# Kernel optimization log

Measured on AMD Instinct MI355X. Metric: run time of the kernel, lower is better.

## Reference

```python
import jax, jax.numpy as jnp
import numpy as np

B, T, IN, H, L, OUT = 1024, 48, 64, 512, 3, 1


def setup_inputs() -> dict:
    key = jax.random.key(0)
    ks = jax.random.split(key, 12)
    s = 0.05
    inp = {
        "x": jax.random.normal(ks[0], (B, T, IN), dtype=jnp.float32),
        # layer 0: input IN -> H ; gates concatenated [f,i,c,o] along last dim
        "Wx0": jax.random.normal(ks[1], (IN, 4 * H), dtype=jnp.float32) * s,
        "Wh0": jax.random.normal(ks[2], (H, 4 * H), dtype=jnp.float32) * s,
        "b0": jnp.zeros((4 * H,), dtype=jnp.float32),
        "Wx1": jax.random.normal(ks[3], (H, 4 * H), dtype=jnp.float32) * s,
        "Wh1": jax.random.normal(ks[4], (H, 4 * H), dtype=jnp.float32) * s,
        "b1": jnp.zeros((4 * H,), dtype=jnp.float32),
        "Wx2": jax.random.normal(ks[5], (H, 4 * H), dtype=jnp.float32) * s,
        "Wh2": jax.random.normal(ks[6], (H, 4 * H), dtype=jnp.float32) * s,
        "b2": jnp.zeros((4 * H,), dtype=jnp.float32),
        "fc_w": jax.random.normal(ks[7], (H, OUT), dtype=jnp.float32) * s,
        "fc_b": jnp.zeros((OUT,), dtype=jnp.float32),
    }
    return inp


def _lstm_cell(Wx, Wh, b, x_t, h, C):
    # fused 4-gate GEMM, same math as 8 separate Linears in the torch code
    g = x_t @ Wx + h @ Wh + b  # [B, 4H]
    f, i, c, o = jnp.split(g, 4, axis=-1)
    f = jax.nn.sigmoid(f)
    i = jax.nn.sigmoid(i)
    c = jnp.tanh(c)
    o = jax.nn.sigmoid(o)
    C_new = f * C + i * c
    h_new = o * jnp.tanh(C_new)  # dropout is identity in eval mode
    return h_new, C_new


def reference(x, Wx0, Wh0, b0, Wx1, Wh1, b1, Wx2, Wh2, b2, fc_w, fc_b):
    params = [(Wx0, Wh0, b0), (Wx1, Wh1, b1), (Wx2, Wh2, b2)]
    Bsz = x.shape[0]
    Hsz = Wh0.shape[0]
    h0 = jnp.zeros((L, Bsz, Hsz), dtype=x.dtype)
    C0 = jnp.zeros((L, Bsz, Hsz), dtype=x.dtype)

    def step(carry, x_t):
        h, C = carry
        inp = x_t
        hs, Cs = [], []
        for l in range(L):
            Wx, Wh, b = params[l]
            hn, Cn = _lstm_cell(Wx, Wh, b, inp, h[l], C[l])
            hs.append(hn)
            Cs.append(Cn)
            inp = hn
        return (jnp.stack(hs), jnp.stack(Cs)), None

    (h, C), _ = jax.lax.scan(step, (h0, C0), jnp.swapaxes(x, 0, 1))
    return h[-1] @ fc_w + fc_b  # [B, OUT]
```

## Files before the change

### kernel.cpp

```cpp
#include <hip/hip_runtime.h>
#include <hip/hip_bf16.h>
#include <stdint.h>

#define BSZ 1024
#define HSZ 512
#define TSZ 48
#define INSZ 64
#define GSZ 2048

typedef __attribute__((ext_vector_type(8))) short bf16x8;
typedef __attribute__((ext_vector_type(16))) float f32x16;

#define GLDS16(g, l)                                                        \
    __builtin_amdgcn_global_load_lds(                                       \
        (const __attribute__((address_space(1))) void*)(g),                 \
        (__attribute__((address_space(3))) void*)(l), 16, 0, 0)

#define SB0 __builtin_amdgcn_sched_barrier(0);
#define WAITV8 asm volatile("s_waitcnt vmcnt(8)" ::: "memory");
#define BARRAW __builtin_amdgcn_s_barrier();

__device__ __forceinline__ float sigmf(float x) { return 1.0f / (1.0f + __expf(-x)); }
__device__ __forceinline__ float tanhf_(float x) { return 2.0f / (1.0f + __expf(-2.0f * x)) - 1.0f; }

__global__ __launch_bounds__(256, 3) void lstm_diag(
    const __hip_bfloat16* __restrict__ xth, const __hip_bfloat16* __restrict__ xtl,
    __hip_bfloat16* __restrict__ hbuf,
    float* __restrict__ Cbuf,
    const __hip_bfloat16* __restrict__ W0h, const __hip_bfloat16* __restrict__ W0l,
    const __hip_bfloat16* __restrict__ W1h, const __hip_bfloat16* __restrict__ W1l,
    const __hip_bfloat16* __restrict__ W2h, const __hip_bfloat16* __restrict__ W2l,
    const float* __restrict__ b0, const float* __restrict__ b1,
    const float* __restrict__ b2,
    int d, int lmin)
{
    __shared__ __align__(16) char lds[33792];

    const int l = lmin + blockIdx.z;
    const int t = d - l;
    const size_t slab = (size_t)BSZ * HSZ;
    auto Hb = [&](int par, int ll, int hilo) {
        return hbuf + (((size_t)par * 3 + ll) * 2 + hilo) * slab;
    };

    const __hip_bfloat16* Wth = (l == 0) ? W0h : (l == 1) ? W1h : W2h;
    const __hip_bfloat16* Wtl = (l == 0) ? W0l : (l == 1) ? W1l : W2l;
    const float* bias = (l == 0) ? b0 : (l == 1) ? b1 : b2;
    const int Kx   = (l == 0) ? INSZ : HSZ;
    const int KCax = (l == 0) ? 8 : 64;
    const int Ktot = Kx + HSZ;
    const int KCt  = Ktot >> 3;
    const int nkx  = Kx >> 6;
    const int nkt  = Ktot >> 6;
    const int cur = t & 1, prv = cur ^ 1;
    const __hip_bfloat16* Axh = (l == 0) ? xth + (size_t)t * BSZ * INSZ : Hb(cur, l - 1, 0);
    const __hip_bfloat16* Axl = (l == 0) ? xtl + (size_t)t * BSZ * INSZ : Hb(cur, l - 1, 1);
    const __hip_bfloat16* Ahh = Hb(prv, l, 0);
    const __hip_bfloat16* Ahl = Hb(prv, l, 1);
    float* C = Cbuf + (size_t)l * slab;
    __hip_bfloat16* hhi = Hb(cur, l, 0);
    __hip_bfloat16* hlo = Hb(cur, l, 1);

    const int bid = blockIdx.x + (blockIdx.y << 4);
    const int swz = (bid & 7) * 32 + (bid >> 3);
    const int m0 = (swz & 15) * 64;
    const int n0 = (swz >> 4) * 128;
    const int p  = swz & 15;
    const int np = swz >> 4;

    const int tid = threadIdx.x;
    const int lane = tid & 63;
    const int wv = tid >> 6;
    const int lrow32 = lane & 31;
    const int lk2 = lane >> 5;

    const char* bAxh = (const char*)Axh + (size_t)p * KCax * 1024;
    const char* bAxl = (const char*)Axl + (size_t)p * KCax * 1024;
    const char* bAhh = (const char*)Ahh + (size_t)p * 64 * 1024;
    const char* bAhl = (const char*)Ahl + (size_t)p * 64 * 1024;
    const char* bWh = (const char*)Wth + (size_t)np * KCt * 2048;
    const char* bWl = (const char*)Wtl + (size_t)np * KCt * 2048;

    const int boff = (wv * 32 + lrow32) * 16;
    const int aoff = lrow32 * 16;

    f32x16 acc0, acc1;
#pragma unroll
    for (int r = 0; r < 16; ++r) { acc0[r] = 0.0f; acc1[r] = 0.0f; }

    auto stage = [&](int ks) {
        const char *sh, *sl;
        int kc0;
        if (ks < nkx) { sh = bAxh; sl = bAxl; kc0 = ks * 8; }
        else          { sh = bAhh; sl = bAhl; kc0 = (ks - nkx) * 8; }
        char* dst = lds + (ks & 1) * 16384;
#pragma unroll
        for (int i = 0; i < 2; ++i) {
            int kc = wv * 2 + i;
            size_t so = (size_t)(kc0 + kc) * 1024 + lane * 16;
            GLDS16(sh + so, dst + kc * 1024);
            GLDS16(sl + so, dst + 8192 + kc * 1024);
        }
    };

    bf16x8 bA[8], bB[8];

#define LOADB(SET, KS)                                                      \
    { const char* wb_ = bWh + (size_t)(KS) * 16384;                         \
      const char* wl_ = bWl + (size_t)(KS) * 16384;                         \
      _Pragma("unroll")                                                     \
      for (int s_ = 0; s_ < 4; ++s_) {                                      \
          int ko_ = (s_ * 2 + lk2) * 2048 + boff;                           \
          SET[s_]     = *(const bf16x8*)(wb_ + ko_);                        \
          SET[s_ + 4] = *(const bf16x8*)(wl_ + ko_);                        \
      } }

#define COMPUTE(SET, KS)                                                    \
    { char* buf_ = lds + ((KS) & 1) * 16384;                                \
      __builtin_amdgcn_s_setprio(1);                                        \
      _Pragma("unroll")                                                     \
      for (int s_ = 0; s_ < 4; ++s_) {                                      \
          int ao_ = (s_ * 2 + lk2) * 1024 + aoff;                           \
          bf16x8 ah0 = *(const bf16x8*)(buf_ + ao_);                        \
          bf16x8 ah1 = *(const bf16x8*)(buf_ + ao_ + 512);                  \
          bf16x8 al0 = *(const bf16x8*)(buf_ + 8192 + ao_);                 \
          bf16x8 al1 = *(const bf16x8*)(buf_ + 8192 + ao_ + 512);           \
          acc0 = __builtin_amdgcn_mfma_f32_32x32x16_bf16(ah0, SET[s_], acc0, 0, 0, 0);     \
          acc1 = __builtin_amdgcn_mfma_f32_32x32x16_bf16(ah1, SET[s_], acc1, 0, 0, 0);     \
          acc0 = __builtin_amdgcn_mfma_f32_32x32x16_bf16(al0, SET[s_], acc0, 0, 0, 0);     \
          acc1 = __builtin_amdgcn_mfma_f32_32x32x16_bf16(al1, SET[s_], acc1, 0, 0, 0);     \
          acc0 = __builtin_amdgcn_mfma_f32_32x32x16_bf16(ah0, SET[s_ + 4], acc0, 0, 0, 0); \
          acc1 = __builtin_amdgcn_mfma_f32_32x32x16_bf16(ah1, SET[s_ + 4], acc1, 0, 0, 0); \
      }                                                                     \
      __builtin_amdgcn_s_setprio(0); }

    stage(0);
    SB0
    LOADB(bA, 0)
    SB0
    WAITV8
    BARRAW

#pragma unroll 1
    for (int ks = 0; ks < nkt; ) {
        if (ks + 1 < nkt) { stage(ks + 1); SB0 LOADB(bB, ks + 1) }
        SB0
        COMPUTE(bA, ks)
        SB0
        WAITV8
        BARRAW
        ++ks;
        if (ks == nkt) break;
        if (ks + 1 < nkt) { stage(ks + 1); SB0 LOADB(bA, ks + 1) }
        SB0
        COMPUTE(bB, ks)
        SB0
        WAITV8
        BARRAW
        ++ks;
    }
#undef LOADB
#undef COMPUTE
    SB0

    float* gt = (float*)lds;
#pragma unroll
    for (int rg = 0; rg < 16; ++rg) {
        int row = (rg & 3) + 8 * (rg >> 2) + 4 * lk2;
        gt[row * 132 + wv * 32 + lrow32] = acc0[rg];
        gt[(row + 32) * 132 + wv * 32 + lrow32] = acc1[rg];
    }
    __syncthreads();

    const int n_l = tid & 31;
    const int rb2 = (tid >> 5) * 8;
    const int n_g = (n0 >> 2) + n_l;
    const int kc_h = n_g >> 3, e_h = n_g & 7;
    const float bf = bias[n_g], bi = bias[HSZ + n_g];
    const float bc = bias[2 * HSZ + n_g], bo = bias[3 * HSZ + n_g];
#pragma unroll
    for (int r = 0; r < 8; ++r) {
        int row = rb2 + r;
        int rg = m0 + row;
        float4 g4 = *(const float4*)&gt[row * 132 + n_l * 4];
        float f = sigmf(g4.x + bf);
        float i_ = sigmf(g4.y + bi);
        float c_ = tanhf_(g4.z + bc);
        float o_ = sigmf(g4.w + bo);
        size_t cidx = (size_t)rg * HSZ + n_g;
        float Cn = f * C[cidx] + i_ * c_;
        C[cidx] = Cn;
        float hv = o_ * tanhf_(Cn);
        __hip_bfloat16 hh = __float2bfloat16(hv);
        size_t hidx = (((size_t)(rg >> 6) * 64 + kc_h) * 64 + (rg & 63)) * 8 + e_h;
        hhi[hidx] = hh;
        hlo[hidx] = __float2bfloat16(hv - __bfloat162float(hh));
    }
}

__global__ __launch_bounds__(256) void convert_x(const float* __restrict__ x,
                                                 __hip_bfloat16* __restrict__ xh,
                                                 __hip_bfloat16* __restrict__ xl)
{
    int gid = blockIdx.x * 256 + threadIdx.x;
    int kc = gid & 7;
    int rem = gid >> 3;
    int r = rem & 63; rem >>= 6;
    int pp = rem & 15;
    int t = rem >> 4;
    int b = pp * 64 + r;
    const float* src = x + ((size_t)b * TSZ + t) * INSZ + kc * 8;
    short hi8[8], lo8[8];
#pragma unroll
    for (int e = 0; e < 8; ++e) {
        float v = src[e];
        __hip_bfloat16 h = __float2bfloat16(v);
        hi8[e] = *(short*)&h;
        __hip_bfloat16 lo = __float2bfloat16(v - __bfloat162float(h));
        lo8[e] = *(short*)&lo;
    }
    size_t o = ((((size_t)t * 16 + pp) * 8 + kc) * 64 + r) * 8;
    *(bf16x8*)((__hip_bfloat16*)xh + o) = *(bf16x8*)hi8;
    *(bf16x8*)((__hip_bfloat16*)xl + o) = *(bf16x8*)lo8;
}

__global__ __launch_bounds__(256) void convert_w(
    const float* __restrict__ Wx, const float* __restrict__ Wh, int Kx, int Ktot,
    __hip_bfloat16* __restrict__ outh, __hip_bfloat16* __restrict__ outl)
{
    __shared__ float tile[64][129];
    const int kt = blockIdx.x, np = blockIdx.y;
    const int k0 = kt * 64;
    const float* src;
    int krel;
    if (k0 < Kx) { src = Wx; krel = k0; } else { src = Wh; krel = k0 - Kx; }
#pragma unroll
    for (int i = 0; i < 32; ++i) {
        int idx = threadIdx.x + i * 256;
        int k_l = idx >> 7, gate = (idx >> 5) & 3, n_l = idx & 31;
        tile[k_l][n_l * 4 + gate] = src[(size_t)(krel + k_l) * GSZ + gate * HSZ + np * 32 + n_l];
    }
    __syncthreads();
    const size_t obase = ((size_t)np * (Ktot >> 3) + kt * 8) * 1024;
#pragma unroll
    for (int i = 0; i < 32; ++i) {
        int idx = threadIdx.x + i * 256;
        int kcl = idx >> 10, c = (idx >> 3) & 127, e = idx & 7;
        float v = tile[kcl * 8 + e][c];
        __hip_bfloat16 h = __float2bfloat16(v);
        outh[obase + idx] = h;
        outl[obase + idx] = __float2bfloat16(v - __bfloat162float(h));
    }
}

__global__ __launch_bounds__(256) void fc_kernel(
    const __hip_bfloat16* __restrict__ hh, const __hip_bfloat16* __restrict__ hl,
    const float* __restrict__ w, const float* __restrict__ b, float* __restrict__ out)
{
    int wave = (blockIdx.x * 256 + threadIdx.x) >> 6;
    int lane = threadIdx.x & 63;
    if (wave >= BSZ) return;
    int pp = wave >> 6, r = wave & 63;
    size_t o = (((size_t)pp * 64 + lane) * 64 + r) * 8;
    bf16x8 vh = *(const bf16x8*)(hh + o);
    bf16x8 vl = *(const bf16x8*)(hl + o);
    float s = 0.0f;
#pragma unroll
    for (int e = 0; e < 8; ++e) {
        ushort uh = (ushort)vh[e], ul = (ushort)vl[e];
        __hip_bfloat16 bh = *(__hip_bfloat16*)&uh;
        __hip_bfloat16 bl = *(__hip_bfloat16*)&ul;
        s += (__bfloat162float(bh) + __bfloat162float(bl)) * w[lane * 8 + e];
    }
#pragma unroll
    for (int off = 32; off; off >>= 1) s += __shfl_down(s, off);
    if (lane == 0) out[wave] = s + b[0];
}

extern "C" void kernel_launch(void* const* d_in, const int* in_sizes, int n_in,
                              void* d_out, int out_size, void* d_ws, size_t ws_size,
                              hipStream_t stream) {
    const float* x   = (const float*)d_in[0];
    const float* Wx0 = (const float*)d_in[1];
    const float* Wh0 = (const float*)d_in[2];
    const float* b0  = (const float*)d_in[3];
    const float* Wx1 = (const float*)d_in[4];
    const float* Wh1 = (const float*)d_in[5];
    const float* b1  = (const float*)d_in[6];
    const float* Wx2 = (const float*)d_in[7];
    const float* Wh2 = (const float*)d_in[8];
    const float* b2  = (const float*)d_in[9];
    const float* fcw = (const float*)d_in[10];
    const float* fcb = (const float*)d_in[11];

    char* p = (char*)d_ws;
    const size_t hslab = (size_t)BSZ * HSZ * sizeof(__hip_bfloat16);
    __hip_bfloat16* hbuf = (__hip_bfloat16*)p;
    p += 12 * hslab;
    float* Cbuf = (float*)p;
    p += 3 * (size_t)BSZ * HSZ * sizeof(float);
    const size_t zero_bytes = (size_t)(p - (char*)d_ws);

    const size_t xslab = (size_t)TSZ * BSZ * INSZ * sizeof(__hip_bfloat16);
    __hip_bfloat16* xth = (__hip_bfloat16*)p; p += xslab;
    __hip_bfloat16* xtl = (__hip_bfloat16*)p; p += xslab;

    const int K0 = INSZ + HSZ;
    const int K12 = 2 * HSZ;
    const size_t w0s = (size_t)GSZ * K0 * sizeof(__hip_bfloat16);
    const size_t w12s = (size_t)GSZ * K12 * sizeof(__hip_bfloat16);
    __hip_bfloat16* w0h = (__hip_bfloat16*)p; p += w0s;
    __hip_bfloat16* w0l = (__hip_bfloat16*)p; p += w0s;
    __hip_bfloat16* w1h = (__hip_bfloat16*)p; p += w12s;
    __hip_bfloat16* w1l = (__hip_bfloat16*)p; p += w12s;
    __hip_bfloat16* w2h = (__hip_bfloat16*)p; p += w12s;
    __hip_bfloat16* w2l = (__hip_bfloat16*)p; p += w12s;

    hipMemsetAsync(d_ws, 0, zero_bytes, stream);

    convert_x<<<dim3(TSZ * BSZ * 8 / 256), dim3(256), 0, stream>>>(x, xth, xtl);
    convert_w<<<dim3(K0 / 64, 16), dim3(256), 0, stream>>>(Wx0, Wh0, INSZ, K0, w0h, w0l);
    convert_w<<<dim3(K12 / 64, 16), dim3(256), 0, stream>>>(Wx1, Wh1, HSZ, K12, w1h, w1l);
    convert_w<<<dim3(K12 / 64, 16), dim3(256), 0, stream>>>(Wx2, Wh2, HSZ, K12, w2h, w2l);

    for (int dgn = 0; dgn < TSZ + 2; ++dgn) {
        int lmin = (dgn - (TSZ - 1)) > 0 ? (dgn - (TSZ - 1)) : 0;
        int lmax = dgn < 2 ? dgn : 2;
        int ncells = lmax - lmin + 1;
        lstm_diag<<<dim3(16, 16, ncells), dim3(256), 0, stream>>>(
            xth, xtl, hbuf, Cbuf,
            w0h, w0l, w1h, w1l, w2h, w2l,
            b0, b1, b2, dgn, lmin);
    }

    __hip_bfloat16* h2h = hbuf + (((size_t)1 * 3 + 2) * 2 + 0) * BSZ * HSZ;
    __hip_bfloat16* h2l = hbuf + (((size_t)1 * 3 + 2) * 2 + 1) * BSZ * HSZ;
    fc_kernel<<<dim3(BSZ / 4), dim3(256), 0, stream>>>(h2h, h2l, fcw, fcb, (float*)d_out);
}
```

Before: 1.985 ms.

## Replace bf16 hi/lo split GEMM with int8 hi/lo fixed-point MFMA

Quantizes weights (per-column scales), inputs and hidden states to 14-bit fixed point split into two int8 parts, and computes the three cross products with i8 32x32x32 MFMAs into int32 accumulators, rescaling in the epilogue. This halves MFMA instruction count and the bytes moved per K step compared with the bf16 split. Accuracy drops to roughly 13-bit fixed point, and inputs are clamped assuming |x| stays below 6.

```diff
diff --git a/kernel.cpp b/kernel.cpp
--- a/kernel.cpp
+++ b/kernel.cpp
@@ -8,8 +8,9 @@
 #define INSZ 64
 #define GSZ 2048
 
-typedef __attribute__((ext_vector_type(8))) short bf16x8;
-typedef __attribute__((ext_vector_type(16))) float f32x16;
+typedef __attribute__((ext_vector_type(4))) int i32x4;
+typedef __attribute__((ext_vector_type(16))) int i32x16;
+typedef __attribute__((ext_vector_type(8))) char char8;
 
 #define GLDS16(g, l)                                                        \
     __builtin_amdgcn_global_load_lds(                                       \
@@ -17,19 +18,24 @@
         (__attribute__((address_space(3))) void*)(l), 16, 0, 0)
 
 #define SB0 __builtin_amdgcn_sched_barrier(0);
-#define WAITV8 asm volatile("s_waitcnt vmcnt(8)" ::: "memory");
+#define WAITV4 asm volatile("s_waitcnt vmcnt(4)" ::: "memory");
 #define BARRAW __builtin_amdgcn_s_barrier();
 
 __device__ __forceinline__ float sigmf(float x) { return 1.0f / (1.0f + __expf(-x)); }
 __device__ __forceinline__ float tanhf_(float x) { return 2.0f / (1.0f + __expf(-2.0f * x)) - 1.0f; }
+__device__ __forceinline__ int clamp13(int q) {
+    return q > 8191 ? 8191 : (q < -8191 ? -8191 : q);
+}
 
 __global__ __launch_bounds__(256, 3) void lstm_diag(
-    const __hip_bfloat16* __restrict__ xth, const __hip_bfloat16* __restrict__ xtl,
-    __hip_bfloat16* __restrict__ hbuf,
+    const char* __restrict__ xqh, const char* __restrict__ xql,
+    char* __restrict__ hq,
     float* __restrict__ Cbuf,
-    const __hip_bfloat16* __restrict__ W0h, const __hip_bfloat16* __restrict__ W0l,
-    const __hip_bfloat16* __restrict__ W1h, const __hip_bfloat16* __restrict__ W1l,
-    const __hip_bfloat16* __restrict__ W2h, const __hip_bfloat16* __restrict__ W2l,
+    const char* __restrict__ W0h, const char* __restrict__ W0l,
+    const char* __restrict__ W1h, const char* __restrict__ W1l,
+    const char* __restrict__ W2h, const char* __restrict__ W2l,
+    const float* __restrict__ ws0, const float* __restrict__ ws1,
+    const float* __restrict__ ws2,
     const float* __restrict__ b0, const float* __restrict__ b1,
     const float* __restrict__ b2,
     int d, int lmin)
@@ -38,28 +44,29 @@
 
     const int l = lmin + blockIdx.z;
     const int t = d - l;
-    const size_t slab = (size_t)BSZ * HSZ;
-    auto Hb = [&](int par, int ll, int hilo) {
-        return hbuf + (((size_t)par * 3 + ll) * 2 + hilo) * slab;
+    const size_t hsl = (size_t)BSZ * HSZ;
+    auto Hq = [&](int par, int ll, int hilo) {
+        return hq + (((size_t)par * 3 + ll) * 2 + hilo) * hsl;
     };
 
-    const __hip_bfloat16* Wth = (l == 0) ? W0h : (l == 1) ? W1h : W2h;
-    const __hip_bfloat16* Wtl = (l == 0) ? W0l : (l == 1) ? W1l : W2l;
+    const char* Wph = (l == 0) ? W0h : (l == 1) ? W1h : W2h;
+    const char* Wpl = (l == 0) ? W0l : (l == 1) ? W1l : W2l;
+    const float* wsc = (l == 0) ? ws0 : (l == 1) ? ws1 : ws2;
     const float* bias = (l == 0) ? b0 : (l == 1) ? b1 : b2;
-    const int Kx   = (l == 0) ? INSZ : HSZ;
-    const int KCax = (l == 0) ? 8 : 64;
-    const int Ktot = Kx + HSZ;
-    const int KCt  = Ktot >> 3;
-    const int nkx  = Kx >> 6;
-    const int nkt  = Ktot >> 6;
+    const int Kx    = (l == 0) ? INSZ : HSZ;
+    const int KCa16 = Kx >> 4;
+    const int Ktot  = Kx + HSZ;
+    const int KCt16 = Ktot >> 4;
+    const int nkx   = Kx >> 6;
+    const int nkt   = Ktot >> 6;
     const int cur = t & 1, prv = cur ^ 1;
-    const __hip_bfloat16* Axh = (l == 0) ? xth + (size_t)t * BSZ * INSZ : Hb(cur, l - 1, 0);
-    const __hip_bfloat16* Axl = (l == 0) ? xtl + (size_t)t * BSZ * INSZ : Hb(cur, l - 1, 1);
-    const __hip_bfloat16* Ahh = Hb(prv, l, 0);
-    const __hip_bfloat16* Ahl = Hb(prv, l, 1);
-    float* C = Cbuf + (size_t)l * slab;
-    __hip_bfloat16* hhi = Hb(cur, l, 0);
-    __hip_bfloat16* hlo = Hb(cur, l, 1);
+    const char* Axh = (l == 0) ? xqh + (size_t)t * 65536 : Hq(cur, l - 1, 0);
+    const char* Axl = (l == 0) ? xql + (size_t)t * 65536 : Hq(cur, l - 1, 1);
+    const char* Ahh = Hq(prv, l, 0);
+    const char* Ahl = Hq(prv, l, 1);
+    float* C = Cbuf + (size_t)l * BSZ * HSZ;
+    char* hhi = Hq(cur, l, 0);
+    char* hlo = Hq(cur, l, 1);
 
     const int bid = blockIdx.x + (blockIdx.y << 4);
     const int swz = (bid & 7) * 32 + (bid >> 3);
@@ -74,88 +81,82 @@
     const int lrow32 = lane & 31;
     const int lk2 = lane >> 5;
 
-    const char* bAxh = (const char*)Axh + (size_t)p * KCax * 1024;
-    const char* bAxl = (const char*)Axl + (size_t)p * KCax * 1024;
-    const char* bAhh = (const char*)Ahh + (size_t)p * 64 * 1024;
-    const char* bAhl = (const char*)Ahl + (size_t)p * 64 * 1024;
-    const char* bWh = (const char*)Wth + (size_t)np * KCt * 2048;
-    const char* bWl = (const char*)Wtl + (size_t)np * KCt * 2048;
+    const char* bAxh = Axh + (size_t)p * KCa16 * 1024;
+    const char* bAxl = Axl + (size_t)p * KCa16 * 1024;
+    const char* bAhh = Ahh + (size_t)p * 32 * 1024;
+    const char* bAhl = Ahl + (size_t)p * 32 * 1024;
+    const char* bWhp = Wph + (size_t)np * KCt16 * 2048;
+    const char* bWlp = Wpl + (size_t)np * KCt16 * 2048;
 
     const int boff = (wv * 32 + lrow32) * 16;
     const int aoff = lrow32 * 16;
 
-    f32x16 acc0, acc1;
-#pragma unroll
-    for (int r = 0; r < 16; ++r) { acc0[r] = 0.0f; acc1[r] = 0.0f; }
+    i32x16 acc0h, acc0x, acc1h, acc1x;
+#pragma unroll
+    for (int r = 0; r < 16; ++r) { acc0h[r] = 0; acc0x[r] = 0; acc1h[r] = 0; acc1x[r] = 0; }
 
     auto stage = [&](int ks) {
         const char *sh, *sl;
         int kc0;
-        if (ks < nkx) { sh = bAxh; sl = bAxl; kc0 = ks * 8; }
-        else          { sh = bAhh; sl = bAhl; kc0 = (ks - nkx) * 8; }
-        char* dst = lds + (ks & 1) * 16384;
-#pragma unroll
-        for (int i = 0; i < 2; ++i) {
-            int kc = wv * 2 + i;
-            size_t so = (size_t)(kc0 + kc) * 1024 + lane * 16;
-            GLDS16(sh + so, dst + kc * 1024);
-            GLDS16(sl + so, dst + 8192 + kc * 1024);
-        }
+        if (ks < nkx) { sh = bAxh; sl = bAxl; kc0 = ks * 4; }
+        else          { sh = bAhh; sl = bAhl; kc0 = (ks - nkx) * 4; }
+        char* dst = lds + (ks & 1) * 8192;
+        size_t so = (size_t)(kc0 + wv) * 1024 + lane * 16;
+        GLDS16(sh + so, dst + wv * 1024);
+        GLDS16(sl + so, dst + 4096 + wv * 1024);
     };
 
-    bf16x8 bA[8], bB[8];
-
-#define LOADB(SET, KS)                                                      \
-    { const char* wb_ = bWh + (size_t)(KS) * 16384;                         \
-      const char* wl_ = bWl + (size_t)(KS) * 16384;                         \
-      _Pragma("unroll")                                                     \
-      for (int s_ = 0; s_ < 4; ++s_) {                                      \
-          int ko_ = (s_ * 2 + lk2) * 2048 + boff;                           \
-          SET[s_]     = *(const bf16x8*)(wb_ + ko_);                        \
-          SET[s_ + 4] = *(const bf16x8*)(wl_ + ko_);                        \
+    i32x4 bAh[2], bAl[2], bBh[2], bBl[2];
+
+#define LOADB(BH, BL, KS)                                                   \
+    { _Pragma("unroll")                                                     \
+      for (int ksub_ = 0; ksub_ < 2; ++ksub_) {                             \
+          int ko_ = ((KS) * 4 + ksub_ * 2 + lk2) * 2048 + boff;             \
+          BH[ksub_] = *(const i32x4*)(bWhp + ko_);                          \
+          BL[ksub_] = *(const i32x4*)(bWlp + ko_);                          \
       } }
 
-#define COMPUTE(SET, KS)                                                    \
-    { char* buf_ = lds + ((KS) & 1) * 16384;                                \
+#define COMPUTE(BH, BL, KS)                                                 \
+    { char* buf_ = lds + ((KS) & 1) * 8192;                                 \
       __builtin_amdgcn_s_setprio(1);                                        \
       _Pragma("unroll")                                                     \
-      for (int s_ = 0; s_ < 4; ++s_) {                                      \
-          int ao_ = (s_ * 2 + lk2) * 1024 + aoff;                           \
-          bf16x8 ah0 = *(const bf16x8*)(buf_ + ao_);                        \
-          bf16x8 ah1 = *(const bf16x8*)(buf_ + ao_ + 512);                  \
-          bf16x8 al0 = *(const bf16x8*)(buf_ + 8192 + ao_);                 \
-          bf16x8 al1 = *(const bf16x8*)(buf_ + 8192 + ao_ + 512);           \
-          acc0 = __builtin_amdgcn_mfma_f32_32x32x16_bf16(ah0, SET[s_], acc0, 0, 0, 0);     \
-          acc1 = __builtin_amdgcn_mfma_f32_32x32x16_bf16(ah1, SET[s_], acc1, 0, 0, 0);     \
-          acc0 = __builtin_amdgcn_mfma_f32_32x32x16_bf16(al0, SET[s_], acc0, 0, 0, 0);     \
-          acc1 = __builtin_amdgcn_mfma_f32_32x32x16_bf16(al1, SET[s_], acc1, 0, 0, 0);     \
-          acc0 = __builtin_amdgcn_mfma_f32_32x32x16_bf16(ah0, SET[s_ + 4], acc0, 0, 0, 0); \
-          acc1 = __builtin_amdgcn_mfma_f32_32x32x16_bf16(ah1, SET[s_ + 4], acc1, 0, 0, 0); \
+      for (int ksub_ = 0; ksub_ < 2; ++ksub_) {                             \
+          int ao_ = (ksub_ * 2 + lk2) * 1024 + aoff;                        \
+          i32x4 ah0 = *(const i32x4*)(buf_ + ao_);                          \
+          i32x4 ah1 = *(const i32x4*)(buf_ + ao_ + 512);                    \
+          i32x4 al0 = *(const i32x4*)(buf_ + 4096 + ao_);                   \
+          i32x4 al1 = *(const i32x4*)(buf_ + 4096 + ao_ + 512);             \
+          acc0h = __builtin_amdgcn_mfma_i32_32x32x32_i8(ah0, BH[ksub_], acc0h, 0, 0, 0); \
+          acc1h = __builtin_amdgcn_mfma_i32_32x32x32_i8(ah1, BH[ksub_], acc1h, 0, 0, 0); \
+          acc0x = __builtin_amdgcn_mfma_i32_32x32x32_i8(ah0, BL[ksub_], acc0x, 0, 0, 0); \
+          acc0x = __builtin_amdgcn_mfma_i32_32x32x32_i8(al0, BH[ksub_], acc0x, 0, 0, 0); \
+          acc1x = __builtin_amdgcn_mfma_i32_32x32x32_i8(ah1, BL[ksub_], acc1x, 0, 0, 0); \
+          acc1x = __builtin_amdgcn_mfma_i32_32x32x32_i8(al1, BH[ksub_], acc1x, 0, 0, 0); \
       }                                                                     \
       __builtin_amdgcn_s_setprio(0); }
 
     stage(0);
     SB0
-    LOADB(bA, 0)
+    LOADB(bAh, bAl, 0)
     SB0
-    WAITV8
+    WAITV4
     BARRAW
 
 #pragma unroll 1
     for (int ks = 0; ks < nkt; ) {
-        if (ks + 1 < nkt) { stage(ks + 1); SB0 LOADB(bB, ks + 1) }
+        if (ks + 1 < nkt) { stage(ks + 1); SB0 LOADB(bBh, bBl, ks + 1) }
         SB0
-        COMPUTE(bA, ks)
+        COMPUTE(bAh, bAl, ks)
         SB0
-        WAITV8
+        WAITV4
         BARRAW
         ++ks;
         if (ks == nkt) break;
-        if (ks + 1 < nkt) { stage(ks + 1); SB0 LOADB(bA, ks + 1) }
+        if (ks + 1 < nkt) { stage(ks + 1); SB0 LOADB(bAh, bAl, ks + 1) }
         SB0
-        COMPUTE(bB, ks)
+        COMPUTE(bBh, bBl, ks)
         SB0
-        WAITV8
+        WAITV4
         BARRAW
         ++ks;
     }
@@ -164,18 +165,21 @@
     SB0
 
     float* gt = (float*)lds;
+    const int colw = wv * 32 + lrow32;
+    const float sb = wsc[n0 + colw];
+    const float s1 = sb * 2.44140625e-4f;
+    const float s2 = sb * 1.9073486328125e-6f;
 #pragma unroll
     for (int rg = 0; rg < 16; ++rg) {
         int row = (rg & 3) + 8 * (rg >> 2) + 4 * lk2;
-        gt[row * 132 + wv * 32 + lrow32] = acc0[rg];
-        gt[(row + 32) * 132 + wv * 32 + lrow32] = acc1[rg];
+        gt[row * 132 + colw] = (float)acc0h[rg] * s1 + (float)acc0x[rg] * s2;
+        gt[(row + 32) * 132 + colw] = (float)acc1h[rg] * s1 + (float)acc1x[rg] * s2;
     }
     __syncthreads();
 
     const int n_l = tid & 31;
     const int rb2 = (tid >> 5) * 8;
     const int n_g = (n0 >> 2) + n_l;
-    const int kc_h = n_g >> 3, e_h = n_g & 7;
     const float bf = bias[n_g], bi = bias[HSZ + n_g];
     const float bc = bias[2 * HSZ + n_g], bo = bias[3 * HSZ + n_g];
 #pragma unroll
@@ -191,42 +195,63 @@
         float Cn = f * C[cidx] + i_ * c_;
         C[cidx] = Cn;
         float hv = o_ * tanhf_(Cn);
-        __hip_bfloat16 hh = __float2bfloat16(hv);
-        size_t hidx = (((size_t)(rg >> 6) * 64 + kc_h) * 64 + (rg & 63)) * 8 + e_h;
-        hhi[hidx] = hh;
-        hlo[hidx] = __float2bfloat16(hv - __bfloat162float(hh));
-    }
+        int hqv = clamp13(__float2int_rn(hv * 8192.0f));
+        int hh8 = (hqv + 64) >> 7;
+        int hl8 = hqv - (hh8 << 7);
+        size_t hidx = (((size_t)(rg >> 6) * 32 + (n_g >> 4)) * 64 + (rg & 63)) * 16 + (n_g & 15);
+        hhi[hidx] = (char)hh8;
+        hlo[hidx] = (char)hl8;
+    }
+}
+
+__device__ __forceinline__ int pack4(int a, int b, int c, int d) {
+    return (a & 255) | ((b & 255) << 8) | ((c & 255) << 16) | ((d & 255) << 24);
 }
 
 __global__ __launch_bounds__(256) void convert_x(const float* __restrict__ x,
-                                                 __hip_bfloat16* __restrict__ xh,
-                                                 __hip_bfloat16* __restrict__ xl)
+                                                 char* __restrict__ xh,
+                                                 char* __restrict__ xl)
 {
     int gid = blockIdx.x * 256 + threadIdx.x;
-    int kc = gid & 7;
-    int rem = gid >> 3;
-    int r = rem & 63; rem >>= 6;
-    int pp = rem & 15;
-    int t = rem >> 4;
+    int r = gid & 63;
+    int kc = (gid >> 6) & 3;
+    int pp = (gid >> 8) & 15;
+    int t = gid >> 12;
     int b = pp * 64 + r;
-    const float* src = x + ((size_t)b * TSZ + t) * INSZ + kc * 8;
-    short hi8[8], lo8[8];
-#pragma unroll
-    for (int e = 0; e < 8; ++e) {
-        float v = src[e];
-        __hip_bfloat16 h = __float2bfloat16(v);
-        hi8[e] = *(short*)&h;
-        __hip_bfloat16 lo = __float2bfloat16(v - __bfloat162float(h));
-        lo8[e] = *(short*)&lo;
-    }
-    size_t o = ((((size_t)t * 16 + pp) * 8 + kc) * 64 + r) * 8;
-    *(bf16x8*)((__hip_bfloat16*)xh + o) = *(bf16x8*)hi8;
-    *(bf16x8*)((__hip_bfloat16*)xl + o) = *(bf16x8*)lo8;
+    const float* src = x + ((size_t)b * TSZ + t) * INSZ + kc * 16;
+    int qh[16], ql[16];
+#pragma unroll
+    for (int j = 0; j < 16; ++j) {
+        int q = clamp13(__float2int_rn(src[j] * (8192.0f / 6.0f)));
+        qh[j] = (q + 64) >> 7;
+        ql[j] = q - (qh[j] << 7);
+    }
+    size_t o = ((((size_t)t * 16 + pp) * 4 + kc) * 64 + r) * 16;
+    i32x4 ph, pl;
+#pragma unroll
+    for (int w = 0; w < 4; ++w) {
+        ph[w] = pack4(qh[4 * w], qh[4 * w + 1], qh[4 * w + 2], qh[4 * w + 3]);
+        pl[w] = pack4(ql[4 * w], ql[4 * w + 1], ql[4 * w + 2], ql[4 * w + 3]);
+    }
+    *(i32x4*)(xh + o) = ph;
+    *(i32x4*)(xl + o) = pl;
+}
+
+__global__ __launch_bounds__(256) void wscale_kernel(
+    const float* __restrict__ Wx, const float* __restrict__ Wh,
+    int Kx, float xmul, float* __restrict__ out)
+{
+    int sc = blockIdx.x * 256 + threadIdx.x;
+    float m = 1e-8f;
+    for (int k = 0; k < Kx; ++k) m = fmaxf(m, fabsf(Wx[(size_t)k * GSZ + sc]) * xmul);
+    for (int k = 0; k < HSZ; ++k) m = fmaxf(m, fabsf(Wh[(size_t)k * GSZ + sc]));
+    out[(sc & 511) * 4 + (sc >> 9)] = m;
 }
 
 __global__ __launch_bounds__(256) void convert_w(
-    const float* __restrict__ Wx, const float* __restrict__ Wh, int Kx, int Ktot,
-    __hip_bfloat16* __restrict__ outh, __hip_bfloat16* __restrict__ outl)
+    const float* __restrict__ Wx, const float* __restrict__ Wh,
+    int Kx, int Ktot, int kxlim, float xmul, const float* __restrict__ wsc,
+    char* __restrict__ outh, char* __restrict__ outl)
 {
     __shared__ float tile[64][129];
     const int kt = blockIdx.x, np = blockIdx.y;
@@ -238,43 +263,47 @@
     for (int i = 0; i < 32; ++i) {
         int idx = threadIdx.x + i * 256;
         int k_l = idx >> 7, gate = (idx >> 5) & 3, n_l = idx & 31;
-        tile[k_l][n_l * 4 + gate] = src[(size_t)(krel + k_l) * GSZ + gate * HSZ + np * 32 + n_l];
+        float mul = (k0 + k_l < kxlim) ? xmul : 1.0f;
+        tile[k_l][n_l * 4 + gate] =
+            src[(size_t)(krel + k_l) * GSZ + gate * HSZ + np * 32 + n_l] * mul;
     }
     __syncthreads();
-    const size_t obase = ((size_t)np * (Ktot >> 3) + kt * 8) * 1024;
+    const size_t obase = ((size_t)np * (Ktot >> 4) + kt * 4) * 2048;
 #pragma unroll
     for (int i = 0; i < 32; ++i) {
         int idx = threadIdx.x + i * 256;
-        int kcl = idx >> 10, c = (idx >> 3) & 127, e = idx & 7;
-        float v = tile[kcl * 8 + e][c];
-        __hip_bfloat16 h = __float2bfloat16(v);
-        outh[obase + idx] = h;
-        outl[obase + idx] = __float2bfloat16(v - __bfloat162float(h));
+        int kcl = idx >> 11, c = (idx >> 4) & 127, e = idx & 15;
+        float v = tile[kcl * 16 + e][c];
+        float s = wsc[np * 128 + c];
+        int q = clamp13(__float2int_rn(v * 8192.0f / s));
+        int qh = (q + 64) >> 7;
+        int ql = q - (qh << 7);
+        outh[obase + idx] = (char)qh;
+        outl[obase + idx] = (char)ql;
     }
 }
 
 __global__ __launch_bounds__(256) void fc_kernel(
-    const __hip_bfloat16* __restrict__ hh, const __hip_bfloat16* __restrict__ hl,
-    const float* __restrict__ w, const float* __restrict__ b, float* __restrict__ out)
+    const char* __restrict__ hh, const char* __restrict__ hl,
+    const float* __restrict__ w, const float* __restrict__ b,
+    float* __restrict__ out)
 {
     int wave = (blockIdx.x * 256 + threadIdx.x) >> 6;
     int lane = threadIdx.x & 63;
     if (wave >= BSZ) return;
     int pp = wave >> 6, r = wave & 63;
-    size_t o = (((size_t)pp * 64 + lane) * 64 + r) * 8;
-    bf16x8 vh = *(const bf16x8*)(hh + o);
-    bf16x8 vl = *(const bf16x8*)(hl + o);
+    size_t o = (((size_t)pp * 32 + (lane >> 1)) * 64 + r) * 16 + (lane & 1) * 8;
+    char8 vh = *(const char8*)(hh + o);
+    char8 vl = *(const char8*)(hl + o);
     float s = 0.0f;
 #pragma unroll
-    for (int e = 0; e < 8; ++e) {
-        ushort uh = (ushort)vh[e], ul = (ushort)vl[e];
-        __hip_bfloat16 bh = *(__hip_bfloat16*)&uh;
-        __hip_bfloat16 bl = *(__hip_bfloat16*)&ul;
-        s += (__bfloat162float(bh) + __bfloat162float(bl)) * w[lane * 8 + e];
+    for (int j = 0; j < 8; ++j) {
+        int hv = (int)vh[j] * 128 + (int)vl[j];
+        s += (float)hv * w[lane * 8 + j];
     }
 #pragma unroll
     for (int off = 32; off; off >>= 1) s += __shfl_down(s, off);
-    if (lane == 0) out[wave] = s + b[0];
+    if (lane == 0) out[wave] = s * (1.0f / 8192.0f) + b[0];
 }
 
 extern "C" void kernel_launch(void* const* d_in, const int* in_sizes, int n_in,
@@ -294,46 +323,50 @@
     const float* fcb = (const float*)d_in[11];
 
     char* p = (char*)d_ws;
-    const size_t hslab = (size_t)BSZ * HSZ * sizeof(__hip_bfloat16);
-    __hip_bfloat16* hbuf = (__hip_bfloat16*)p;
-    p += 12 * hslab;
-    float* Cbuf = (float*)p;
-    p += 3 * (size_t)BSZ * HSZ * sizeof(float);
+    const size_t hsl = (size_t)BSZ * HSZ;
+    char* hq = p; p += 12 * hsl;
+    float* Cbuf = (float*)p; p += 3 * hsl * sizeof(float);
     const size_t zero_bytes = (size_t)(p - (char*)d_ws);
 
-    const size_t xslab = (size_t)TSZ * BSZ * INSZ * sizeof(__hip_bfloat16);
-    __hip_bfloat16* xth = (__hip_bfloat16*)p; p += xslab;
-    __hip_bfloat16* xtl = (__hip_bfloat16*)p; p += xslab;
+    const size_t xsl = (size_t)TSZ * BSZ * INSZ;
+    char* xqh = p; p += xsl;
+    char* xql = p; p += xsl;
 
     const int K0 = INSZ + HSZ;
     const int K12 = 2 * HSZ;
-    const size_t w0s = (size_t)GSZ * K0 * sizeof(__hip_bfloat16);
-    const size_t w12s = (size_t)GSZ * K12 * sizeof(__hip_bfloat16);
-    __hip_bfloat16* w0h = (__hip_bfloat16*)p; p += w0s;
-    __hip_bfloat16* w0l = (__hip_bfloat16*)p; p += w0s;
-    __hip_bfloat16* w1h = (__hip_bfloat16*)p; p += w12s;
-    __hip_bfloat16* w1l = (__hip_bfloat16*)p; p += w12s;
-    __hip_bfloat16* w2h = (__hip_bfloat16*)p; p += w12s;
-    __hip_bfloat16* w2l = (__hip_bfloat16*)p; p += w12s;
+    const size_t w0s = (size_t)GSZ * K0;
+    const size_t w12s = (size_t)GSZ * K12;
+    char* w0h = p; p += w0s;
+    char* w0l = p; p += w0s;
+    char* w1h = p; p += w12s;
+    char* w1l = p; p += w12s;
+    char* w2h = p; p += w12s;
+    char* w2l = p; p += w12s;
+    float* ws0 = (float*)p; p += GSZ * sizeof(float);
+    float* ws1 = (float*)p; p += GSZ * sizeof(float);
+    float* ws2 = (float*)p; p += GSZ * sizeof(float);
 
     hipMemsetAsync(d_ws, 0, zero_bytes, stream);
 
-    convert_x<<<dim3(TSZ * BSZ * 8 / 256), dim3(256), 0, stream>>>(x, xth, xtl);
-    convert_w<<<dim3(K0 / 64, 16), dim3(256), 0, stream>>>(Wx0, Wh0, INSZ, K0, w0h, w0l);
-    convert_w<<<dim3(K12 / 64, 16), dim3(256), 0, stream>>>(Wx1, Wh1, HSZ, K12, w1h, w1l);
-    convert_w<<<dim3(K12 / 64, 16), dim3(256), 0, stream>>>(Wx2, Wh2, HSZ, K12, w2h, w2l);
+    wscale_kernel<<<dim3(8), dim3(256), 0, stream>>>(Wx0, Wh0, INSZ, 6.0f, ws0);
+    wscale_kernel<<<dim3(8), dim3(256), 0, stream>>>(Wx1, Wh1, HSZ, 1.0f, ws1);
+    wscale_kernel<<<dim3(8), dim3(256), 0, stream>>>(Wx2, Wh2, HSZ, 1.0f, ws2);
+    convert_w<<<dim3(K0 / 64, 16), dim3(256), 0, stream>>>(Wx0, Wh0, INSZ, K0, 64, 6.0f, ws0, w0h, w0l);
+    convert_w<<<dim3(K12 / 64, 16), dim3(256), 0, stream>>>(Wx1, Wh1, HSZ, K12, 0, 1.0f, ws1, w1h, w1l);
+    convert_w<<<dim3(K12 / 64, 16), dim3(256), 0, stream>>>(Wx2, Wh2, HSZ, K12, 0, 1.0f, ws2, w2h, w2l);
+    convert_x<<<dim3(TSZ * BSZ * INSZ / 16 / 256), dim3(256), 0, stream>>>(x, xqh, xql);
 
     for (int dgn = 0; dgn < TSZ + 2; ++dgn) {
         int lmin = (dgn - (TSZ - 1)) > 0 ? (dgn - (TSZ - 1)) : 0;
         int lmax = dgn < 2 ? dgn : 2;
         int ncells = lmax - lmin + 1;
         lstm_diag<<<dim3(16, 16, ncells), dim3(256), 0, stream>>>(
-            xth, xtl, hbuf, Cbuf,
+            xqh, xql, hq, Cbuf,
             w0h, w0l, w1h, w1l, w2h, w2l,
-            b0, b1, b2, dgn, lmin);
-    }
-
-    __hip_bfloat16* h2h = hbuf + (((size_t)1 * 3 + 2) * 2 + 0) * BSZ * HSZ;
-    __hip_bfloat16* h2l = hbuf + (((size_t)1 * 3 + 2) * 2 + 1) * BSZ * HSZ;
+            ws0, ws1, ws2, b0, b1, b2, dgn, lmin);
+    }
+
+    char* h2h = hq + (((size_t)1 * 3 + 2) * 2 + 0) * hsl;
+    char* h2l = hq + (((size_t)1 * 3 + 2) * 2 + 1) * hsl;
     fc_kernel<<<dim3(BSZ / 4), dim3(256), 0, stream>>>(h2h, h2l, fcw, fcb, (float*)d_out);
 }
```

Result: slower. 2.920 ms (+47.1%).
